# Optimization experiments

Hardware: AMD Instinct MI355X
Metric: run time of the kernel (lower is better)

Reference implementation:

```python
import jax, jax.numpy as jnp
import numpy as np

D_MODEL = 1024
NHEAD = 16
D_HEAD = D_MODEL // NHEAD


def setup_inputs() -> dict:
    key = jax.random.key(0)
    ks = jax.random.split(key, 9)
    B, S = 2, 2048
    scale = 1.0 / np.sqrt(D_MODEL)
    x = jax.random.normal(ks[0], (B, S, D_MODEL), dtype=jnp.float32)
    Wq = jax.random.normal(ks[1], (D_MODEL, D_MODEL), dtype=jnp.float32) * scale
    Wk = jax.random.normal(ks[2], (D_MODEL, D_MODEL), dtype=jnp.float32) * scale
    Wv = jax.random.normal(ks[3], (D_MODEL, D_MODEL), dtype=jnp.float32) * scale
    Wo = jax.random.normal(ks[4], (D_MODEL, D_MODEL), dtype=jnp.float32) * scale
    bq = jax.random.normal(ks[5], (D_MODEL,), dtype=jnp.float32) * 0.01
    bk = jax.random.normal(ks[6], (D_MODEL,), dtype=jnp.float32) * 0.01
    bv = jax.random.normal(ks[7], (D_MODEL,), dtype=jnp.float32) * 0.01
    bo = jax.random.normal(ks[8], (D_MODEL,), dtype=jnp.float32) * 0.01
    return {"x": x, "Wq": Wq, "bq": bq, "Wk": Wk, "bk": bk,
            "Wv": Wv, "bv": bv, "Wo": Wo, "bo": bo}


def reference(x, Wq, bq, Wk, bk, Wv, bv, Wo, bo):
    B, S, D = x.shape
    H, Dh = NHEAD, D_HEAD
    # projections; weights stored as (in, out) so y = x @ W + b
    def split_heads(t):  # [B,S,D] -> [B,H,S,Dh]
        return t.reshape(B, S, H, Dh).transpose(0, 2, 1, 3)
    q = split_heads(x @ Wq + bq)
    k = split_heads(x @ Wk + bk)
    v = split_heads(x @ Wv + bv)
    scale = 1.0 / jnp.sqrt(jnp.asarray(Dh, dtype=x.dtype))
    attn = jnp.einsum("bhqd,bhkd->bhqk", q, k) * scale  # [B,H,S,S]
    attn = jax.nn.softmax(attn, axis=-1)
    out = jnp.einsum("bhqk,bhkd->bhqd", attn, v)  # [B,H,S,Dh]
    out = out.transpose(0, 2, 1, 3).reshape(B, S, D)
    return out @ Wo + bo
```

## Files before the change

kernel.cpp:

```cpp
#include <hip/hip_runtime.h>
#include <hip/hip_bf16.h>
#include <stdint.h>
#include <stddef.h>

typedef __bf16 b16;
typedef __bf16 b16x4 __attribute__((ext_vector_type(4)));
typedef __bf16 b16x8 __attribute__((ext_vector_type(8)));
typedef float  f32x4 __attribute__((ext_vector_type(4)));

#define LOG2E 1.4426950408889634f
#define QSCALE (0.125f * LOG2E)

#if __has_builtin(__builtin_amdgcn_exp2f)
#define EXP2F(x) __builtin_amdgcn_exp2f(x)
#else
#define EXP2F(x) exp2f(x)
#endif

typedef __attribute__((address_space(1))) void gvoid;
typedef __attribute__((address_space(3))) void svoid;

__device__ __forceinline__ void async_cp16(void* lds, const void* g) {
    __builtin_amdgcn_global_load_lds((gvoid*)(void*)g, (svoid*)lds, 16, 0, 0);
}

#define SW(r) ((((r) & 7)) ^ (((r) >> 1) & 4))

__global__ __launch_bounds__(256) void k_prep(const float* __restrict__ x,
                                              const float* __restrict__ Wq,
                                              const float* __restrict__ Wk,
                                              const float* __restrict__ Wv,
                                              const float* __restrict__ Wo,
                                              b16* __restrict__ Xb,
                                              b16* __restrict__ WtQKV,
                                              b16* __restrict__ Wot) {
    const int z = blockIdx.z;
    if (z == 4) {
        const int blk = blockIdx.y * 32 + blockIdx.x;
        const float* src = x + (size_t)blk * 4096;
        b16* dst = Xb + (size_t)blk * 4096;
#pragma unroll
        for (int c = 0; c < 4; ++c) {
            const int i = c * 1024 + threadIdx.x * 4;
            float4 v = *(const float4*)(src + i);
            b16x4 o = { (b16)v.x, (b16)v.y, (b16)v.z, (b16)v.w };
            *(b16x4*)(dst + i) = o;
        }
        return;
    }
    __shared__ float t[32][33];
    const float* W = (z == 0) ? Wq : (z == 1) ? Wk : (z == 2) ? Wv : Wo;
    const int k0 = blockIdx.x * 32, n0 = blockIdx.y * 32;
    const int tr = threadIdx.x >> 3, tc4 = (threadIdx.x & 7) * 4;
    float4 v = *(const float4*)(W + (size_t)(k0 + tr) * 1024 + n0 + tc4);
    t[tr][tc4 + 0] = v.x; t[tr][tc4 + 1] = v.y;
    t[tr][tc4 + 2] = v.z; t[tr][tc4 + 3] = v.w;
    __syncthreads();
    b16* dst = (z < 3) ? (WtQKV + ((size_t)z << 20)) : Wot;
    b16x4 o = { (b16)t[tc4 + 0][tr], (b16)t[tc4 + 1][tr],
                (b16)t[tc4 + 2][tr], (b16)t[tc4 + 3][tr] };
    *(b16x4*)(dst + (size_t)(n0 + tr) * 1024 + k0 + tc4) = o;
}

__device__ __forceinline__ void gemm128_core(const b16* __restrict__ Ag,
                                             const b16* __restrict__ Bg,
                                             b16* As, b16* Bs, int tid,
                                             f32x4 acc[4][4]) {
    const int lane = tid & 63, wave = tid >> 6;
    const int wm = wave & 1, wn = wave >> 1;
    const int quad = lane >> 4, lc = lane & 15;
    const int ci0 = tid, ci1 = tid + 256;
    const b16* a0 = Ag + (ci0 >> 2) * 1024 + (ci0 & 3) * 8;
    const b16* a1 = Ag + (ci1 >> 2) * 1024 + (ci1 & 3) * 8;
    const b16* b0 = Bg + (ci0 >> 2) * 1024 + (ci0 & 3) * 8;
    const b16* b1 = Bg + (ci1 >> 2) * 1024 + (ci1 & 3) * 8;

#define GSTAGE(BUF, K0) do {                                   \
        async_cp16(As + (BUF) * 4096 + ci0 * 8, a0 + (K0));    \
        async_cp16(As + (BUF) * 4096 + ci1 * 8, a1 + (K0));    \
        async_cp16(Bs + (BUF) * 4096 + ci0 * 8, b0 + (K0));    \
        async_cp16(Bs + (BUF) * 4096 + ci1 * 8, b1 + (K0));    \
    } while (0)

    auto gcompute = [&](int buf) {
        const b16* Al = As + buf * 4096;
        const b16* Bl = Bs + buf * 4096;
        b16x8 af[4], bfr[4];
#pragma unroll
        for (int mt = 0; mt < 4; ++mt)
            af[mt] = *(const b16x8*)(Al + (wm * 64 + mt * 16 + lc) * 32 + quad * 8);
#pragma unroll
        for (int nt = 0; nt < 4; ++nt)
            bfr[nt] = *(const b16x8*)(Bl + (wn * 64 + nt * 16 + lc) * 32 + quad * 8);
#pragma unroll
        for (int mt = 0; mt < 4; ++mt)
#pragma unroll
            for (int nt = 0; nt < 4; ++nt)
                acc[mt][nt] = __builtin_amdgcn_mfma_f32_16x16x32_bf16(
                    af[mt], bfr[nt], acc[mt][nt], 0, 0, 0);
    };

    GSTAGE(0, 0);
    for (int k0 = 0; k0 < 1024; k0 += 64) {
        GSTAGE(1, k0 + 32);
        asm volatile("s_waitcnt vmcnt(4)" ::: "memory");
        __builtin_amdgcn_s_barrier();
        __builtin_amdgcn_sched_barrier(0);
        gcompute(0);
        __builtin_amdgcn_sched_barrier(0);
        __builtin_amdgcn_s_barrier();
        if (k0 + 64 < 1024) {
            GSTAGE(0, k0 + 64);
            asm volatile("s_waitcnt vmcnt(4)" ::: "memory");
        } else {
            asm volatile("s_waitcnt vmcnt(0)" ::: "memory");
        }
        __builtin_amdgcn_s_barrier();
        __builtin_amdgcn_sched_barrier(0);
        gcompute(1);
        __builtin_amdgcn_sched_barrier(0);
        __builtin_amdgcn_s_barrier();
    }
#undef GSTAGE
}

__global__ __launch_bounds__(256, 2) void k_gemm_qkv(
    const b16* __restrict__ A, const b16* __restrict__ Bt,
    const float* __restrict__ bq, const float* __restrict__ bk,
    const float* __restrict__ bv,
    b16* __restrict__ Qg, b16* __restrict__ Kg, b16* __restrict__ Vtg) {
    __shared__ __align__(16) b16 LB[16384];
    b16* As = LB;
    b16* Bs = LB + 8192;
    char* Tb = (char*)LB;
    const int bm = blockIdx.x, bn = blockIdx.y;
    const int tid = threadIdx.x;
    const int lane = tid & 63, wave = tid >> 6;
    const int wm = wave & 1, wn = wave >> 1;
    const int quad = lane >> 4, lc = lane & 15;

    f32x4 acc[4][4] = {};
    gemm128_core(A + (size_t)(bm * 128) * 1024, Bt + (size_t)(bn * 128) * 1024,
                 As, Bs, tid, acc);

    const int mat = bn >> 3;
    const float* bp = (mat == 0) ? bq : (mat == 1) ? bk : bv;
    const float scl = (mat == 0) ? QSCALE : 1.0f;

#pragma unroll
    for (int nt = 0; nt < 4; ++nt) {
        const int ln = wn * 64 + nt * 16 + lc;
        const float bval = bp[(bn * 128 + ln) & 1023];
#pragma unroll
        for (int mt = 0; mt < 4; ++mt) {
            const int lm = wm * 64 + mt * 16 + quad * 4;
            if (mat == 2) {
                b16x4 o;
#pragma unroll
                for (int r = 0; r < 4; ++r) o[r] = (b16)(acc[mt][nt][r] + bval);
                const int byte = ln * 256 + (((lm >> 3) ^ (ln & 15)) << 4) + (lm & 7) * 2;
                *(b16x4*)(Tb + byte) = o;
            } else {
#pragma unroll
                for (int r = 0; r < 4; ++r) {
                    const int row = lm + r;
                    const int byte = row * 256 + (((ln >> 3) ^ (row & 15)) << 4) + (ln & 7) * 2;
                    *(b16*)(Tb + byte) = (b16)((acc[mt][nt][r] + bval) * scl);
                }
            }
        }
    }
    __syncthreads();

    const int chunk = tid & 7, hr0 = tid >> 3;
    const int b = bm >> 4;
    const int s_blk = (bm * 128) & 2047;
#pragma unroll
    for (int p = 0; p < 8; ++p) {
        const int hr = p * 32 + hr0;
        const int row = hr >> 1, half = hr & 1;
        const int c2 = (half * 8 + chunk) ^ (row & 15);
        b16x8 v = *(const b16x8*)(Tb + row * 256 + c2 * 16);
        if (mat == 2) {
            const int cm = (bn * 128 + row) & 1023;
            const int h = cm >> 6, dh = cm & 63;
            *(b16x8*)(Vtg + (size_t)((b * 16 + h) * 64 + dh) * 2048 +
                      s_blk + half * 64 + chunk * 8) = v;
        } else {
            const int s = s_blk + row;
            const int cm = (bn * 128 + half * 64 + chunk * 8) & 1023;
            const int h = cm >> 6, dh = cm & 63;
            b16* dst = (mat == 0) ? Qg : Kg;
            *(b16x8*)(dst + ((size_t)(b * 16 + h) * 2048 + s) * 64 + dh) = v;
        }
    }
}

__global__ __launch_bounds__(256, 4) void k_flash(
    const b16* __restrict__ Qg, const b16* __restrict__ Kg,
    const b16* __restrict__ Vtg, b16* __restrict__ AO) {
    __shared__ __align__(16) b16 Ks[2 * 64 * 64];
    __shared__ __align__(16) b16 Vs[2 * 64 * 64];
    __shared__ float Lred[4][16];

    const int bid = blockIdx.x;
    const int qb = bid >> 5;
    const int bh = bid & 31;

    const int tid = threadIdx.x, lane = tid & 63, wave = tid >> 6;
    const int quad = lane >> 4, lc = lane & 15;

    const b16* Kbh = Kg + (size_t)bh * 2048 * 64;
    const b16* Vbh = Vtg + (size_t)bh * 64 * 2048;

    const int ci0 = tid, ci1 = tid + 256;
    const int r0 = ci0 >> 3, gc0 = (ci0 & 7) ^ SW(r0);
    const int r1 = ci1 >> 3, gc1 = (ci1 & 7) ^ SW(r1);
    const b16* pK0 = Kbh + r0 * 64 + gc0 * 8;
    const b16* pK1 = Kbh + r1 * 64 + gc1 * 8;
    const b16* pV0 = Vbh + (size_t)r0 * 2048 + gc0 * 8;
    const b16* pV1 = Vbh + (size_t)r1 * 2048 + gc1 * 8;

#define FSTAGE(BUF) do {                                   \
        async_cp16(Ks + (BUF) * 4096 + ci0 * 8, pK0);      \
        async_cp16(Ks + (BUF) * 4096 + ci1 * 8, pK1);      \
        async_cp16(Vs + (BUF) * 4096 + ci0 * 8, pV0);      \
        async_cp16(Vs + (BUF) * 4096 + ci1 * 8, pV1);      \
        pK0 += 4096; pK1 += 4096; pV0 += 64; pV1 += 64;    \
    } while (0)

    FSTAGE(0);

    const b16* Qbase = Qg + ((size_t)bh * 2048 + qb * 64 + wave * 16) * 64;
    b16x8 qf0 = *(const b16x8*)(Qbase + lc * 64 + quad * 8);
    b16x8 qf1 = *(const b16x8*)(Qbase + lc * 64 + 32 + quad * 8);

    f32x4 oacc[4] = {};
    float lsum = 0.f;

    auto flash_tile = [&](const b16* Kc, const b16* Vc) {
#pragma unroll
        for (int ks = 0; ks < 2; ++ks) {
            b16x8 pf;
#pragma unroll
            for (int t = 0; t < 2; ++t) {
                const int krow = ks * 32 + (lc >> 2) * 8 + t * 4 + (lc & 3);
                b16x8 kf0 = *(const b16x8*)(Kc + krow * 64 + ((0 * 4 + quad) ^ SW(krow)) * 8);
                b16x8 kf1 = *(const b16x8*)(Kc + krow * 64 + ((1 * 4 + quad) ^ SW(krow)) * 8);
                f32x4 s = {};
                __builtin_amdgcn_s_setprio(1);
                s = __builtin_amdgcn_mfma_f32_16x16x32_bf16(kf0, qf0, s, 0, 0, 0);
                s = __builtin_amdgcn_mfma_f32_16x16x32_bf16(kf1, qf1, s, 0, 0, 0);
                __builtin_amdgcn_s_setprio(0);
                float e0 = EXP2F(s[0]), e1 = EXP2F(s[1]);
                float e2 = EXP2F(s[2]), e3 = EXP2F(s[3]);
                lsum += (e0 + e1) + (e2 + e3);
                pf[t * 4 + 0] = (b16)e0;
                pf[t * 4 + 1] = (b16)e1;
                pf[t * 4 + 2] = (b16)e2;
                pf[t * 4 + 3] = (b16)e3;
            }
            b16x8 vf[4];
#pragma unroll
            for (int dt = 0; dt < 4; ++dt) {
                const int row = dt * 16 + lc;
                vf[dt] = *(const b16x8*)(Vc + row * 64 + ((ks * 4 + quad) ^ SW(row)) * 8);
            }
            __builtin_amdgcn_s_setprio(1);
#pragma unroll
            for (int dt = 0; dt < 4; ++dt)
                oacc[dt] = __builtin_amdgcn_mfma_f32_16x16x32_bf16(
                    pf, vf[dt], oacc[dt], 0, 0, 0);
            __builtin_amdgcn_s_setprio(0);
        }
    };

    for (int kt = 0; kt < 32; kt += 2) {
        FSTAGE(1);
        asm volatile("s_waitcnt vmcnt(4)" ::: "memory");
        __builtin_amdgcn_s_barrier();
        __builtin_amdgcn_sched_barrier(0);
        flash_tile(Ks, Vs);
        __builtin_amdgcn_sched_barrier(0);
        __builtin_amdgcn_s_barrier();
        if (kt + 2 < 32) {
            FSTAGE(0);
            asm volatile("s_waitcnt vmcnt(4)" ::: "memory");
        } else {
            asm volatile("s_waitcnt vmcnt(0)" ::: "memory");
        }
        __builtin_amdgcn_s_barrier();
        __builtin_amdgcn_sched_barrier(0);
        flash_tile(Ks + 4096, Vs + 4096);
        __builtin_amdgcn_sched_barrier(0);
        __builtin_amdgcn_s_barrier();
    }
#undef FSTAGE

    lsum += __shfl_xor(lsum, 16, 64);
    lsum += __shfl_xor(lsum, 32, 64);

    if (quad == 0) Lred[wave][lc] = lsum;
    const int b = bh >> 4, h = bh & 15;
#pragma unroll
    for (int r = 0; r < 4; ++r) {
        const float inv = 1.0f / Lred[wave][quad * 4 + r];
        const int s = qb * 64 + wave * 16 + quad * 4 + r;
#pragma unroll
        for (int dt = 0; dt < 4; ++dt)
            AO[(size_t)(b * 2048 + s) * 1024 + h * 64 + dt * 16 + lc] =
                (b16)(oacc[dt][r] * inv);
    }
}

__global__ __launch_bounds__(256, 2) void k_gemm_out(
    const b16* __restrict__ A, const b16* __restrict__ Bt,
    const float* __restrict__ bo, float* __restrict__ out) {
    __shared__ __align__(16) b16 As[2 * 128 * 32];
    __shared__ __align__(16) b16 Bs[2 * 128 * 32];
    const int bm = blockIdx.x, bn = blockIdx.y;
    const int tid = threadIdx.x;
    const int lane = tid & 63, wave = tid >> 6;
    const int wm = wave & 1, wn = wave >> 1;
    const int quad = lane >> 4, lc = lane & 15;

    f32x4 acc[4][4] = {};
    gemm128_core(A + (size_t)(bm * 128) * 1024, Bt + (size_t)(bn * 128) * 1024,
                 As, Bs, tid, acc);

#pragma unroll
    for (int nt = 0; nt < 4; ++nt) {
        const int n = bn * 128 + wn * 64 + nt * 16 + lc;
        const float bval = bo[n];
#pragma unroll
        for (int mt = 0; mt < 4; ++mt) {
            const int m0 = bm * 128 + wm * 64 + mt * 16 + quad * 4;
#pragma unroll
            for (int r = 0; r < 4; ++r)
                out[(size_t)(m0 + r) * 1024 + n] = acc[mt][nt][r] + bval;
        }
    }
}

extern "C" void kernel_launch(void* const* d_in, const int* in_sizes, int n_in,
                              void* d_out, int out_size, void* d_ws, size_t ws_size,
                              hipStream_t stream) {
    const float* x  = (const float*)d_in[0];
    const float* Wq = (const float*)d_in[1];
    const float* bq = (const float*)d_in[2];
    const float* Wk = (const float*)d_in[3];
    const float* bk = (const float*)d_in[4];
    const float* Wv = (const float*)d_in[5];
    const float* bv = (const float*)d_in[6];
    const float* Wo = (const float*)d_in[7];
    const float* bo = (const float*)d_in[8];
    float* out = (float*)d_out;

    char* ws = (char*)d_ws;
    const size_t MB = 1024 * 1024;
    b16* Xb  = (b16*)(ws);
    b16* AO  = (b16*)(ws);
    b16* WtQ = (b16*)(ws + 8 * MB);
    b16* Wot = (b16*)(ws + 14 * MB);
    b16* Qg  = (b16*)(ws + 16 * MB);
    b16* Kg  = (b16*)(ws + 24 * MB);
    b16* Vtg = (b16*)(ws + 32 * MB);

    k_prep<<<dim3(32, 32, 5), 256, 0, stream>>>(x, Wq, Wk, Wv, Wo, Xb, WtQ, Wot);
    k_gemm_qkv<<<dim3(32, 24), 256, 0, stream>>>(Xb, WtQ, bq, bk, bv, Qg, Kg, Vtg);
    k_flash<<<dim3(1024), 256, 0, stream>>>(Qg, Kg, Vtg, AO);
    k_gemm_out<<<dim3(32, 8), 256, 0, stream>>>(AO, Wot, bo, out);
}
```

Before: 190.9 us.

## Triple-buffer GEMM LDS pipeline with priority-boosted MFMA phases

```diff
diff --git a/kernel.cpp b/kernel.cpp
--- a/kernel.cpp
+++ b/kernel.cpp
@@ -82,56 +82,55 @@
         async_cp16(Bs + (BUF) * 4096 + ci1 * 8, b1 + (K0));    \
     } while (0)
 
-    auto gcompute = [&](int buf) {
-        const b16* Al = As + buf * 4096;
-        const b16* Bl = Bs + buf * 4096;
-        b16x8 af[4], bfr[4];
-#pragma unroll
-        for (int mt = 0; mt < 4; ++mt)
-            af[mt] = *(const b16x8*)(Al + (wm * 64 + mt * 16 + lc) * 32 + quad * 8);
-#pragma unroll
-        for (int nt = 0; nt < 4; ++nt)
-            bfr[nt] = *(const b16x8*)(Bl + (wn * 64 + nt * 16 + lc) * 32 + quad * 8);
-#pragma unroll
-        for (int mt = 0; mt < 4; ++mt)
-#pragma unroll
-            for (int nt = 0; nt < 4; ++nt)
-                acc[mt][nt] = __builtin_amdgcn_mfma_f32_16x16x32_bf16(
-                    af[mt], bfr[nt], acc[mt][nt], 0, 0, 0);
-    };
+#define GSTEP(BUF, SBUF, SK0, VM, DOSTAGE) do {                          \
+        if (DOSTAGE) GSTAGE(SBUF, SK0);                                  \
+        asm volatile("s_waitcnt vmcnt(" #VM ")" ::: "memory");           \
+        __builtin_amdgcn_s_barrier();                                    \
+        __builtin_amdgcn_sched_barrier(0);                               \
+        b16x8 af[4], bfr[4];                                             \
+        const b16* Al = As + (BUF) * 4096;                               \
+        const b16* Bl = Bs + (BUF) * 4096;                               \
+        _Pragma("unroll")                                                \
+        for (int mt = 0; mt < 4; ++mt)                                   \
+            af[mt] = *(const b16x8*)(Al + (wm * 64 + mt * 16 + lc) * 32 + quad * 8); \
+        _Pragma("unroll")                                                \
+        for (int nt = 0; nt < 4; ++nt)                                   \
+            bfr[nt] = *(const b16x8*)(Bl + (wn * 64 + nt * 16 + lc) * 32 + quad * 8); \
+        asm volatile("s_waitcnt lgkmcnt(0)" ::: "memory");               \
+        __builtin_amdgcn_sched_barrier(0);                               \
+        __builtin_amdgcn_s_barrier();                                    \
+        __builtin_amdgcn_s_setprio(1);                                   \
+        _Pragma("unroll")                                                \
+        for (int mt = 0; mt < 4; ++mt)                                   \
+            _Pragma("unroll")                                            \
+            for (int nt = 0; nt < 4; ++nt)                               \
+                acc[mt][nt] = __builtin_amdgcn_mfma_f32_16x16x32_bf16(   \
+                    af[mt], bfr[nt], acc[mt][nt], 0, 0, 0);              \
+        __builtin_amdgcn_s_setprio(0);                                   \
+    } while (0)
 
     GSTAGE(0, 0);
-    for (int k0 = 0; k0 < 1024; k0 += 64) {
-        GSTAGE(1, k0 + 32);
-        asm volatile("s_waitcnt vmcnt(4)" ::: "memory");
-        __builtin_amdgcn_s_barrier();
-        __builtin_amdgcn_sched_barrier(0);
-        gcompute(0);
-        __builtin_amdgcn_sched_barrier(0);
-        __builtin_amdgcn_s_barrier();
-        if (k0 + 64 < 1024) {
-            GSTAGE(0, k0 + 64);
-            asm volatile("s_waitcnt vmcnt(4)" ::: "memory");
-        } else {
-            asm volatile("s_waitcnt vmcnt(0)" ::: "memory");
-        }
-        __builtin_amdgcn_s_barrier();
-        __builtin_amdgcn_sched_barrier(0);
-        gcompute(1);
-        __builtin_amdgcn_sched_barrier(0);
-        __builtin_amdgcn_s_barrier();
-    }
+    GSTAGE(1, 32);
+    for (int i = 0; i < 10; ++i) {
+        const int kb = 96 * i;
+        GSTEP(0, 2, kb + 64, 8, 1);
+        GSTEP(1, 0, kb + 96, 8, 1);
+        GSTEP(2, 1, kb + 128, 8, 1);
+    }
+    GSTEP(0, 0, 0, 4, 0);
+    GSTEP(1, 0, 0, 0, 0);
+#undef GSTEP
 #undef GSTAGE
 }
 
-__global__ __launch_bounds__(256, 2) void k_gemm_qkv(
+__global__ __launch_bounds__(256, 3) void k_gemm_qkv(
     const b16* __restrict__ A, const b16* __restrict__ Bt,
     const float* __restrict__ bq, const float* __restrict__ bk,
     const float* __restrict__ bv,
     b16* __restrict__ Qg, b16* __restrict__ Kg, b16* __restrict__ Vtg) {
-    __shared__ __align__(16) b16 LB[16384];
+    __shared__ __align__(16) b16 LB[24576];
     b16* As = LB;
-    b16* Bs = LB + 8192;
+    b16* Bs = LB + 12288;
     char* Tb = (char*)LB;
     const int bm = blockIdx.x, bn = blockIdx.y;
     const int tid = threadIdx.x;
@@ -313,11 +312,11 @@
     }
 }
 
-__global__ __launch_bounds__(256, 2) void k_gemm_out(
+__global__ __launch_bounds__(256, 3) void k_gemm_out(
     const b16* __restrict__ A, const b16* __restrict__ Bt,
     const float* __restrict__ bo, float* __restrict__ out) {
-    __shared__ __align__(16) b16 As[2 * 128 * 32];
-    __shared__ __align__(16) b16 Bs[2 * 128 * 32];
+    __shared__ __align__(16) b16 As[3 * 128 * 32];
+    __shared__ __align__(16) b16 Bs[3 * 128 * 32];
     const int bm = blockIdx.x, bn = blockIdx.y;
     const int tid = threadIdx.x;
     const int lane = tid & 63, wave = tid >> 6;
```

New measurement: 189.6 us. No clear change (-0.7%).
